# Performance work log

Measured on AMD Instinct MI355X. Metric: run time of the kernel, lower is better.

The kernel has to match this reference:

```python
import jax, jax.numpy as jnp
import numpy as np
from jax.scipy.special import logsumexp

B = 2048       # anchors
P = 4          # positives per anchor (constant -> ragged list collapses to [B,P])
D = 256        # embed dim
N_NEG = 32768  # shared negative bank
TEMPERATURE = 0.05
ALPHA = 0.1
EPS = 1e-12    # F.normalize eps


def _l2norm(x):
    n = jnp.sqrt(jnp.sum(x * x, axis=-1, keepdims=True))
    return x / jnp.maximum(n, EPS)


def setup_inputs() -> dict:
    key = jax.random.key(0)
    k1, k2, k3 = jax.random.split(key, 3)
    return {
        "anchor_embeddings": jax.random.normal(k1, (B, D), jnp.float32),
        "positive_embeddings": jax.random.normal(k2, (B * P, D), jnp.float32),
        "negative_embeddings": jax.random.normal(k3, (N_NEG, D), jnp.float32),
        "num_positives_per_anchor": jnp.full((B,), P, dtype=jnp.int32),
    }


def reference(anchor_embeddings, positive_embeddings, negative_embeddings,
              num_positives_per_anchor):
    a = _l2norm(anchor_embeddings)                       # [B, D]
    p = _l2norm(positive_embeddings).reshape(B, P, D)    # [B, P, D]
    n = _l2norm(negative_embeddings)                     # [N, D]

    pos_sim = jnp.einsum("bd,bpd->bp", a, p) / TEMPERATURE   # [B, P]
    neg_sim = jnp.einsum("bd,nd->bn", a, n) / TEMPERATURE    # [B, N]  (dominant traffic)
    neg_lse = logsumexp(neg_sim, axis=1)                     # [B]

    # per-(anchor, positive) CE with label 0 over logits [pos_j, neg_sim_i]:
    # loss = logsumexp([pos_j, neg...]) - pos_j = logaddexp(pos_j, neg_lse_i) - pos_j
    pair_loss = jnp.logaddexp(pos_sim, neg_lse[:, None]) - pos_sim   # [B, P]
    counts = num_positives_per_anchor
    pair_mask = jnp.arange(P)[None, :] < counts[:, None]             # [B, P]
    total = jnp.sum(jnp.where(pair_mask, pair_loss, 0.0))

    # weighted-positive term (only for anchors with num_pos > 1)
    w = jax.nn.softmax(pos_sim, axis=1)                  # [B, P]
    wps = jnp.sum(w * pos_sim, axis=1)                   # [B]
    wloss = jnp.logaddexp(wps, neg_lse) - wps            # [B]
    total = total + ALPHA * jnp.sum(jnp.where(counts > 1, wloss, 0.0))

    return total / B
```

## Files before the change

### kernel.cpp

```cpp
#include <hip/hip_runtime.h>
#include <math.h>

constexpr int   B       = 2048;
constexpr int   P       = 4;
constexpr int   D       = 256;
constexpr int   NNEG    = 32768;
constexpr int   NTILES  = NNEG / 64;
constexpr float TEMP    = 0.05f;
constexpr float ALPHA   = 0.1f;
constexpr float EPS     = 1e-12f;
constexpr float INV_T   = 1.0f / TEMP;
constexpr float SCALE_Q = 28.853900817779268f;

typedef __bf16 bf16x8 __attribute__((ext_vector_type(8)));
typedef float  f32x4  __attribute__((ext_vector_type(4)));

__device__ inline unsigned short f2bf(float f) {
  unsigned int u = __float_as_uint(f);
  u = (u + 0x7fffu + ((u >> 16) & 1u)) >> 16;
  return (unsigned short)u;
}


constexpr int NPANEL = (B + NNEG) / 16;
constexpr int LSTR   = 264;

__global__ __launch_bounds__(256) void prep_kernel(
    const float* __restrict__ a,
    const float* __restrict__ pzx,
    const float* __restrict__ n,
    unsigned short* __restrict__ a_bf,
    unsigned short* __restrict__ n_bf,
    float* __restrict__ pos_sim,
    float* __restrict__ loss_acc,
    unsigned int* __restrict__ ticket) {
  if (blockIdx.x == 0 && threadIdx.x == 0) { *loss_acc = 0.0f; *ticket = 0u; }
  const int id   = blockIdx.x;
  const int tid  = threadIdx.x;
  const int wave = tid >> 6;
  const int lane = tid & 63;

  if (id < NPANEL) {
    __shared__ __align__(16) unsigned short sm[16 * LSTR];
    const float* src; unsigned short* dst; int prow; float post;
    if (id < B / 16) { src = a; dst = a_bf; prow = id;          post = SCALE_Q; }
    else             { src = n; dst = n_bf; prow = id - B / 16; post = 1.0f; }

#pragma unroll
    for (int rr = 0; rr < 4; rr++) {
      const int r = wave * 4 + rr;
      float4 v = ((const float4*)(src + ((size_t)prow * 16 + r) * D))[lane];
      float ss = v.x * v.x + v.y * v.y + v.z * v.z + v.w * v.w;
#pragma unroll
      for (int off = 32; off > 0; off >>= 1) ss += __shfl_xor(ss, off, 64);
      float inv = post / fmaxf(sqrtf(ss), EPS);
      ushort4 o;
      o.x = f2bf(v.x * inv); o.y = f2bf(v.y * inv);
      o.z = f2bf(v.z * inv); o.w = f2bf(v.w * inv);
      *(ushort4*)&sm[r * LSTR + lane * 4] = o;
    }
    __syncthreads();

    const int r1 = (2 * tid) & 15;
    const int r2 = (2 * tid + 1) & 15;
    const int k0 = (tid >> 5) * 32 + ((tid >> 3) & 3) * 8;
    uint4 lo = *(const uint4*)&sm[r1 * LSTR + k0];
    uint4 hi = *(const uint4*)&sm[r2 * LSTR + k0];
    uint4* outp = (uint4*)(dst + (size_t)prow * 4096 + tid * 16);
    outp[0] = lo;
    outp[1] = hi;
  } else {
    int pw = (id - NPANEL) * 4 + wave;
    if (pw >= B * P) return;
    int b = pw >> 2;
    float4 av = ((const float4*)(a + (size_t)b * D))[lane];
    float4 pv = ((const float4*)(pzx + (size_t)pw * D))[lane];
    float d  = av.x * pv.x + av.y * pv.y + av.z * pv.z + av.w * pv.w;
    float sa = av.x * av.x + av.y * av.y + av.z * av.z + av.w * av.w;
    float sp = pv.x * pv.x + pv.y * pv.y + pv.z * pv.z + pv.w * pv.w;
#pragma unroll
    for (int off = 32; off > 0; off >>= 1) {
      d  += __shfl_xor(d, off, 64);
      sa += __shfl_xor(sa, off, 64);
      sp += __shfl_xor(sp, off, 64);
    }
    if (lane == 0) {
      float inva = 1.0f / fmaxf(sqrtf(sa), EPS);
      float invp = 1.0f / fmaxf(sqrtf(sp), EPS);
      pos_sim[pw] = d * inva * invp * INV_T;
    }
  }
}

constexpr int BM = 64, BN = 256;

__global__ __launch_bounds__(256, 4) void negsim_mfma_kernel(
    const unsigned short* __restrict__ Af,
    const unsigned short* __restrict__ Nf,
    float* __restrict__ part_s) {
  __shared__ __align__(16) unsigned short As[32 * 512];

  const int tid  = threadIdx.x;
  const int wave = tid >> 6;
  const int lane = tid & 63;

  const int id   = blockIdx.x;
  const int xcd  = id & 7;
  const int j    = id >> 3;
  const int nblk = xcd * 16 + (j & 15);
  const int mblk = j >> 4;
  const int m0   = mblk * BM;
  const int n0   = nblk * BN;

#pragma unroll
  for (int t = 0; t < 8; t++) {
    const int f = wave * 8 + t;
    const int c = f >> 2, p = f & 3;
    __builtin_amdgcn_global_load_lds(
        (const __attribute__((address_space(1))) unsigned int*)
            (Af + (size_t)((m0 >> 4) + p) * 4096 + c * 512 + lane * 8),
        (__attribute__((address_space(3))) unsigned int*)(As + f * 512 + lane * 8),
        16, 0, 0);
  }
  __syncthreads();

  const unsigned short* Bp = Nf + (size_t)((n0 >> 4) + wave * 4) * 4096 + lane * 8;

  f32x4 acc[4][4] = {};
  bf16x8 b0[4], b1[4];

#pragma unroll
  for (int ni = 0; ni < 4; ni++)
    b0[ni] = *(const bf16x8*)(Bp + (size_t)ni * 4096);

#pragma unroll
  for (int c = 0; c < 8; c += 2) {
#pragma unroll
    for (int ni = 0; ni < 4; ni++)
      b1[ni] = *(const bf16x8*)(Bp + (size_t)ni * 4096 + (c + 1) * 512);
    {
      bf16x8 af[4];
#pragma unroll
      for (int mi = 0; mi < 4; mi++)
        af[mi] = *(const bf16x8*)&As[(c * 4 + mi) * 512 + lane * 8];
#pragma unroll
      for (int mi = 0; mi < 4; mi++)
#pragma unroll
        for (int ni = 0; ni < 4; ni++)
          acc[mi][ni] = __builtin_amdgcn_mfma_f32_16x16x32_bf16(
              af[mi], b0[ni], acc[mi][ni], 0, 0, 0);
    }
    if (c + 2 < 8) {
#pragma unroll
      for (int ni = 0; ni < 4; ni++)
        b0[ni] = *(const bf16x8*)(Bp + (size_t)ni * 4096 + (c + 2) * 512);
    }
    {
      bf16x8 af[4];
#pragma unroll
      for (int mi = 0; mi < 4; mi++)
        af[mi] = *(const bf16x8*)&As[((c + 1) * 4 + mi) * 512 + lane * 8];
#pragma unroll
      for (int mi = 0; mi < 4; mi++)
#pragma unroll
        for (int ni = 0; ni < 4; ni++)
          acc[mi][ni] = __builtin_amdgcn_mfma_f32_16x16x32_bf16(
              af[mi], b1[ni], acc[mi][ni], 0, 0, 0);
    }
  }

#pragma unroll
  for (int mi = 0; mi < 4; mi++) {
#pragma unroll
    for (int rr = 0; rr < 4; rr++) {
      float s = __builtin_amdgcn_exp2f(acc[mi][0][rr]) +
                __builtin_amdgcn_exp2f(acc[mi][1][rr]) +
                __builtin_amdgcn_exp2f(acc[mi][2][rr]) +
                __builtin_amdgcn_exp2f(acc[mi][3][rr]);
#pragma unroll
      for (int off = 1; off < 16; off <<= 1) s += __shfl_xor(s, off, 64);
      if ((lane & 15) == 0) {
        int row = m0 + mi * 16 + (lane >> 4) * 4 + rr;
        part_s[(size_t)row * NTILES + (nblk * 4 + wave)] = s;
      }
    }
  }
}

__global__ void loss_kernel(const float* __restrict__ part_s,
                            const float* __restrict__ pos_sim,
                            const int* __restrict__ counts,
                            float* __restrict__ loss_acc,
                            unsigned int* __restrict__ ticket,
                            float* __restrict__ out) {
  const int tid = threadIdx.x;
  const int b   = blockIdx.x * 16 + (tid >> 4);
  const int sub = tid & 15;
  const float* ps = part_s + (size_t)b * NTILES;
  float s = 0.0f;
#pragma unroll
  for (int i = 0; i < NTILES / 16; i++) s += ps[sub + i * 16];
  s += __shfl_xor(s, 1, 64);
  s += __shfl_xor(s, 2, 64);
  s += __shfl_xor(s, 4, 64);
  s += __shfl_xor(s, 8, 64);

  float acc = 0.0f;
  if (sub == 0) {
    float L = logf(s);
    float p0 = pos_sim[b * P + 0], p1 = pos_sim[b * P + 1];
    float p2 = pos_sim[b * P + 2], p3 = pos_sim[b * P + 3];
    int cnt = counts[b];
    float pj[P] = {p0, p1, p2, p3};
#pragma unroll
    for (int jj = 0; jj < P; jj++) {
      if (jj < cnt) {
        float hi = fmaxf(pj[jj], L), lo = fminf(pj[jj], L);
        acc += hi + log1pf(__expf(lo - hi)) - pj[jj];
      }
    }
    float mp = fmaxf(fmaxf(p0, p1), fmaxf(p2, p3));
    float e0 = __expf(p0 - mp), e1 = __expf(p1 - mp);
    float e2 = __expf(p2 - mp), e3 = __expf(p3 - mp);
    float se = e0 + e1 + e2 + e3;
    float wps = (e0 * p0 + e1 * p1 + e2 * p2 + e3 * p3) / se;
    if (cnt > 1) {
      float hi = fmaxf(wps, L), lo = fminf(wps, L);
      acc += ALPHA * (hi + log1pf(__expf(lo - hi)) - wps);
    }
  }
#pragma unroll
  for (int off = 32; off > 0; off >>= 1) acc += __shfl_xor(acc, off, 64);
  __shared__ float sa[4];
  int wid = tid >> 6, lane = tid & 63;
  if (lane == 0) sa[wid] = acc;
  __syncthreads();
  if (tid == 0) {
    atomicAdd(loss_acc, sa[0] + sa[1] + sa[2] + sa[3]);
    __threadfence();
    unsigned int t = atomicAdd(ticket, 1u);
    if (t == (unsigned int)gridDim.x - 1u) {
      float total = atomicAdd(loss_acc, 0.0f);
      out[0] = total / (float)B;
    }
  }
}

extern "C" void kernel_launch(void* const* d_in, const int* in_sizes, int n_in,
                              void* d_out, int out_size, void* d_ws,
                              size_t ws_size, hipStream_t stream) {
  const float* anc    = (const float*)d_in[0];
  const float* pos    = (const float*)d_in[1];
  const float* neg    = (const float*)d_in[2];
  const int*   counts = (const int*)d_in[3];
  float* out = (float*)d_out;

  unsigned short* a_bf = (unsigned short*)d_ws;
  unsigned short* n_bf = a_bf + (size_t)B * D;
  float* part_s  = (float*)(n_bf + (size_t)NNEG * D);
  float* pos_sim = part_s + (size_t)B * NTILES;
  float* loss_acc = pos_sim + B * P;
  unsigned int* ticket = (unsigned int*)(loss_acc + 1);

  prep_kernel<<<NPANEL + B * P / 4, 256, 0, stream>>>(
      anc, pos, neg, a_bf, n_bf, pos_sim, loss_acc, ticket);

  negsim_mfma_kernel<<<4096, 256, 0, stream>>>(a_bf, n_bf, part_s);

  loss_kernel<<<B / 16, 256, 0, stream>>>(part_s, pos_sim, counts,
                                          loss_acc, ticket, out);
}
```

Measured before the change: 137.4 us.

## Switch negative-similarity GEMM operands from bf16 to fp8 MFMA

The prep kernel now quantizes the normalized anchors and negatives to fp8 instead of bf16, and the main GEMM uses the fp8 16x16x32 MFMA. The packed panel layout and LDS staging are reworked for one-byte elements. This halves the operand bytes written by prep and read by the GEMM, and fp8 MFMA has higher throughput. The cost is lower precision. With anchors scaled by about 28.85 before quantization, fp8 error in the logits gets amplified through exp2 and may push the loss outside tolerance.

```diff
diff --git a/kernel.cpp b/kernel.cpp
--- a/kernel.cpp
+++ b/kernel.cpp
@@ -12,14 +12,16 @@
 constexpr float INV_T   = 1.0f / TEMP;
 constexpr float SCALE_Q = 28.853900817779268f;
 
-typedef __bf16 bf16x8 __attribute__((ext_vector_type(8)));
-typedef float  f32x4  __attribute__((ext_vector_type(4)));
+typedef float f32x4 __attribute__((ext_vector_type(4)));
 
 __device__ inline unsigned short f2bf(float f) {
   unsigned int u = __float_as_uint(f);
   u = (u + 0x7fffu + ((u >> 16) & 1u)) >> 16;
   return (unsigned short)u;
 }
+__device__ inline float bf2f(unsigned short u) {
+  return __uint_as_float((unsigned int)u << 16);
+}
 
 
 constexpr int NPANEL = (B + NNEG) / 16;
@@ -29,8 +31,8 @@
     const float* __restrict__ a,
     const float* __restrict__ pzx,
     const float* __restrict__ n,
-    unsigned short* __restrict__ a_bf,
-    unsigned short* __restrict__ n_bf,
+    unsigned char* __restrict__ a_f8,
+    unsigned char* __restrict__ n_f8,
     float* __restrict__ pos_sim,
     float* __restrict__ loss_acc,
     unsigned int* __restrict__ ticket) {
@@ -42,9 +44,9 @@
 
   if (id < NPANEL) {
     __shared__ __align__(16) unsigned short sm[16 * LSTR];
-    const float* src; unsigned short* dst; int prow; float post;
-    if (id < B / 16) { src = a; dst = a_bf; prow = id;          post = SCALE_Q; }
-    else             { src = n; dst = n_bf; prow = id - B / 16; post = 1.0f; }
+    const float* src; unsigned char* dst; int prow; float post;
+    if (id < B / 16) { src = a; dst = a_f8; prow = id;          post = SCALE_Q; }
+    else             { src = n; dst = n_f8; prow = id - B / 16; post = 1.0f; }
 
 #pragma unroll
     for (int rr = 0; rr < 4; rr++) {
@@ -64,11 +66,22 @@
     const int r1 = (2 * tid) & 15;
     const int r2 = (2 * tid + 1) & 15;
     const int k0 = (tid >> 5) * 32 + ((tid >> 3) & 3) * 8;
-    uint4 lo = *(const uint4*)&sm[r1 * LSTR + k0];
-    uint4 hi = *(const uint4*)&sm[r2 * LSTR + k0];
-    uint4* outp = (uint4*)(dst + (size_t)prow * 4096 + tid * 16);
-    outp[0] = lo;
-    outp[1] = hi;
+    const unsigned short* s1 = &sm[r1 * LSTR + k0];
+    const unsigned short* s2 = &sm[r2 * LSTR + k0];
+    uint4 ov;
+    {
+      int w0 = __builtin_amdgcn_cvt_pk_fp8_f32(bf2f(s1[0]), bf2f(s1[1]), 0, false);
+      w0     = __builtin_amdgcn_cvt_pk_fp8_f32(bf2f(s1[2]), bf2f(s1[3]), w0, true);
+      int w1 = __builtin_amdgcn_cvt_pk_fp8_f32(bf2f(s1[4]), bf2f(s1[5]), 0, false);
+      w1     = __builtin_amdgcn_cvt_pk_fp8_f32(bf2f(s1[6]), bf2f(s1[7]), w1, true);
+      int w2 = __builtin_amdgcn_cvt_pk_fp8_f32(bf2f(s2[0]), bf2f(s2[1]), 0, false);
+      w2     = __builtin_amdgcn_cvt_pk_fp8_f32(bf2f(s2[2]), bf2f(s2[3]), w2, true);
+      int w3 = __builtin_amdgcn_cvt_pk_fp8_f32(bf2f(s2[4]), bf2f(s2[5]), 0, false);
+      w3     = __builtin_amdgcn_cvt_pk_fp8_f32(bf2f(s2[6]), bf2f(s2[7]), w3, true);
+      ov.x = (unsigned)w0; ov.y = (unsigned)w1;
+      ov.z = (unsigned)w2; ov.w = (unsigned)w3;
+    }
+    *(uint4*)(dst + (size_t)prow * 4096 + tid * 16) = ov;
   } else {
     int pw = (id - NPANEL) * 4 + wave;
     if (pw >= B * P) return;
@@ -95,10 +108,10 @@
 constexpr int BM = 64, BN = 256;
 
 __global__ __launch_bounds__(256, 4) void negsim_mfma_kernel(
-    const unsigned short* __restrict__ Af,
-    const unsigned short* __restrict__ Nf,
+    const unsigned char* __restrict__ Af,
+    const unsigned char* __restrict__ Nf,
     float* __restrict__ part_s) {
-  __shared__ __align__(16) unsigned short As[32 * 512];
+  __shared__ __align__(16) unsigned char As[32 * 512];
 
   const int tid  = threadIdx.x;
   const int wave = tid >> 6;
@@ -113,58 +126,57 @@
   const int n0   = nblk * BN;
 
 #pragma unroll
-  for (int t = 0; t < 8; t++) {
-    const int f = wave * 8 + t;
-    const int c = f >> 2, p = f & 3;
+  for (int t = 0; t < 4; t++) {
+    const int s = wave * 4 + t;
     __builtin_amdgcn_global_load_lds(
         (const __attribute__((address_space(1))) unsigned int*)
-            (Af + (size_t)((m0 >> 4) + p) * 4096 + c * 512 + lane * 8),
-        (__attribute__((address_space(3))) unsigned int*)(As + f * 512 + lane * 8),
+            (Af + (size_t)((m0 >> 4) + wave) * 4096 + t * 1024 + lane * 16),
+        (__attribute__((address_space(3))) unsigned int*)(As + s * 1024 + lane * 16),
         16, 0, 0);
   }
   __syncthreads();
 
-  const unsigned short* Bp = Nf + (size_t)((n0 >> 4) + wave * 4) * 4096 + lane * 8;
+  const unsigned char* Bp = Nf + (size_t)((n0 >> 4) + wave * 4) * 4096 + lane * 8;
 
   f32x4 acc[4][4] = {};
-  bf16x8 b0[4], b1[4];
+  long b0[4], b1[4];
 
 #pragma unroll
   for (int ni = 0; ni < 4; ni++)
-    b0[ni] = *(const bf16x8*)(Bp + (size_t)ni * 4096);
+    b0[ni] = *(const long*)(Bp + (size_t)ni * 4096);
 
 #pragma unroll
   for (int c = 0; c < 8; c += 2) {
 #pragma unroll
     for (int ni = 0; ni < 4; ni++)
-      b1[ni] = *(const bf16x8*)(Bp + (size_t)ni * 4096 + (c + 1) * 512);
+      b1[ni] = *(const long*)(Bp + (size_t)ni * 4096 + (c + 1) * 512);
     {
-      bf16x8 af[4];
-#pragma unroll
-      for (int mi = 0; mi < 4; mi++)
-        af[mi] = *(const bf16x8*)&As[(c * 4 + mi) * 512 + lane * 8];
+      long af[4];
+#pragma unroll
+      for (int mi = 0; mi < 4; mi++)
+        af[mi] = *(const long*)&As[(mi * 8 + c) * 512 + lane * 8];
 #pragma unroll
       for (int mi = 0; mi < 4; mi++)
 #pragma unroll
         for (int ni = 0; ni < 4; ni++)
-          acc[mi][ni] = __builtin_amdgcn_mfma_f32_16x16x32_bf16(
+          acc[mi][ni] = __builtin_amdgcn_mfma_f32_16x16x32_fp8_fp8(
               af[mi], b0[ni], acc[mi][ni], 0, 0, 0);
     }
     if (c + 2 < 8) {
 #pragma unroll
       for (int ni = 0; ni < 4; ni++)
-        b0[ni] = *(const bf16x8*)(Bp + (size_t)ni * 4096 + (c + 2) * 512);
+        b0[ni] = *(const long*)(Bp + (size_t)ni * 4096 + (c + 2) * 512);
     }
     {
-      bf16x8 af[4];
-#pragma unroll
-      for (int mi = 0; mi < 4; mi++)
-        af[mi] = *(const bf16x8*)&As[((c + 1) * 4 + mi) * 512 + lane * 8];
+      long af[4];
+#pragma unroll
+      for (int mi = 0; mi < 4; mi++)
+        af[mi] = *(const long*)&As[(mi * 8 + c + 1) * 512 + lane * 8];
 #pragma unroll
       for (int mi = 0; mi < 4; mi++)
 #pragma unroll
         for (int ni = 0; ni < 4; ni++)
-          acc[mi][ni] = __builtin_amdgcn_mfma_f32_16x16x32_bf16(
+          acc[mi][ni] = __builtin_amdgcn_mfma_f32_16x16x32_fp8_fp8(
               af[mi], b1[ni], acc[mi][ni], 0, 0, 0);
     }
   }
@@ -255,17 +267,17 @@
   const int*   counts = (const int*)d_in[3];
   float* out = (float*)d_out;
 
-  unsigned short* a_bf = (unsigned short*)d_ws;
-  unsigned short* n_bf = a_bf + (size_t)B * D;
-  float* part_s  = (float*)(n_bf + (size_t)NNEG * D);
+  unsigned char* a_f8 = (unsigned char*)d_ws;
+  unsigned char* n_f8 = a_f8 + (size_t)B * D;
+  float* part_s  = (float*)(n_f8 + (size_t)NNEG * D);
   float* pos_sim = part_s + (size_t)B * NTILES;
   float* loss_acc = pos_sim + B * P;
   unsigned int* ticket = (unsigned int*)(loss_acc + 1);
 
   prep_kernel<<<NPANEL + B * P / 4, 256, 0, stream>>>(
-      anc, pos, neg, a_bf, n_bf, pos_sim, loss_acc, ticket);
-
-  negsim_mfma_kernel<<<4096, 256, 0, stream>>>(a_bf, n_bf, part_s);
+      anc, pos, neg, a_f8, n_f8, pos_sim, loss_acc, ticket);
+
+  negsim_mfma_kernel<<<4096, 256, 0, stream>>>(a_f8, n_f8, part_s);
 
   loss_kernel<<<B / 16, 256, 0, stream>>>(part_s, pos_sim, counts,
                                           loss_acc, ticket, out);
```

Measured after the change: 126.2 us. 1.09x faster.
